# Kernel optimization log

Hardware: AMD Instinct MI355X
Metric: run time of the kernel (lower is better)

Reference implementation:

```python
import jax, jax.numpy as jnp
import numpy as np

GROUP_SIZE = 128  # K-rows sharing one dequant scale


def _dequant(B, s):
    """Unpack int4 (uint4b8: value = nibble - 8) from packed int32 and apply group scales.
    B: [K//8, N] int32, 8 nibbles per word along K (nibble i -> k = 8*row + i).
    s: [K//GROUP_SIZE, N] float scales.
    Returns W: [K, N] float.
    """
    Kp, N = B.shape
    K = Kp * 8
    shifts = (jnp.arange(8, dtype=jnp.int32) * 4)
    # [Kp, 8, N] nibbles -> [K, N]
    nib = (B[:, None, :] >> shifts[None, :, None]) & 0xF
    w = nib.reshape(K, N).astype(s.dtype) - 8.0
    # per-group scaling: groups of GROUP_SIZE consecutive K rows
    w = (w.reshape(K // GROUP_SIZE, GROUP_SIZE, N) * s[:, None, :]).reshape(K, N)
    return w


def setup_inputs() -> dict:
    key = jax.random.key(0)
    k1, k2, k3 = jax.random.split(key, 3)
    M, K, N = 64, 8192, 8192
    x = jax.random.normal(k1, (M, K), dtype=jnp.float32)
    B = jax.random.randint(k2, (K // 8, N), 0, 2147483647, dtype=jnp.int32)
    s = jax.random.uniform(k3, (K // GROUP_SIZE, N), dtype=jnp.float32) * 0.02
    return {"x": x, "B": B, "s": s}


def reference(x, B, s):
    # machete_mm: fused int4 dequant + GEMM; here expressed as dequant then matmul
    w = _dequant(B, s)          # [K, N]
    out = x @ w                 # [M, N]
    return out
```

## Files before the change

### kernel.cpp

```cpp
#include <hip/hip_runtime.h>

typedef _Float16 half2v __attribute__((ext_vector_type(2)));
typedef _Float16 half8  __attribute__((ext_vector_type(8)));
typedef float    floatx4 __attribute__((ext_vector_type(4)));

#define M_DIM 64
#define K_DIM 8192
#define N_DIM 8192
#define NT 64
#define KSB 8
#define CHUNK (K_DIM / (KSB * 4))
#define STEPS (CHUNK / 32)

__global__ __launch_bounds__(256) void permute_x_kernel(
        const float* __restrict__ x, _Float16* __restrict__ xp) {
    const int t  = blockIdx.x * 256 + threadIdx.x;
    const int c  = t & 15;
    const int q  = (t >> 4) & 3;
    const int mt = (t >> 6) & 3;
    const int kb = t >> 8;
    const int m  = mt * 16 + c;
    const int k0 = kb * 32 + q * 8;
    const float* src = x + (size_t)m * K_DIM + k0;
    float4 a = *(const float4*)(src);
    float4 b = *(const float4*)(src + 4);
    union { _Float16 h[8]; float4 f; } u;
    u.h[0] = (_Float16)a.x; u.h[1] = (_Float16)b.x;
    u.h[2] = (_Float16)a.y; u.h[3] = (_Float16)b.y;
    u.h[4] = (_Float16)a.z; u.h[5] = (_Float16)b.z;
    u.h[6] = (_Float16)a.w; u.h[7] = (_Float16)b.w;
    *(float4*)(xp + (size_t)t * 8) = u.f;
}

__device__ __forceinline__ half2v dq_pair(unsigned int bits, half2v sub, half2v sc) {
    union { unsigned int u; half2v h; } cv;
    cv.u = bits;
    return (cv.h - sub) * sc;
}

__global__ __launch_bounds__(256, 3) void machete_mm_kernel(
        const _Float16* __restrict__ xp,
        const unsigned int* __restrict__ Bq,
        const float* __restrict__ s,
        float* __restrict__ partial) {
    __shared__ float red[4][32][65];

    const int tid  = threadIdx.x;
    const int w    = tid >> 6;
    const int lane = tid & 63;
    const int c    = lane & 15;
    const int q    = lane >> 4;
    const int n0   = blockIdx.x * NT;
    const int ci   = blockIdx.y * 4 + w;
    const int kb   = ci * CHUNK;
    const int ncol = n0 + 4 * c;

    floatx4 acc[4][4];
    #pragma unroll
    for (int i = 0; i < 4; ++i)
        #pragma unroll
        for (int j = 0; j < 4; ++j) acc[i][j] = (floatx4)0.0f;

    const half2v c1032 = { (_Float16)1032.0f, (_Float16)1032.0f };
    half2v s2g[2][4];
    #pragma unroll
    for (int g = 0; g < 2; ++g) {
        const float4 s4 = *(const float4*)(s + (size_t)((kb >> 7) + g) * N_DIM + ncol);
        s2g[g][0] = (half2v){ (_Float16)s4.x, (_Float16)s4.x };
        s2g[g][1] = (half2v){ (_Float16)s4.y, (_Float16)s4.y };
        s2g[g][2] = (half2v){ (_Float16)s4.z, (_Float16)s4.z };
        s2g[g][3] = (half2v){ (_Float16)s4.w, (_Float16)s4.w };
    }

    const unsigned int* bq = Bq + (size_t)((kb >> 3) + q) * N_DIM + ncol;
    const _Float16*     ap = xp + (size_t)(kb >> 5) * 2048 + lane * 8;

    uint4 bbuf[2];
    half8 abuf[2][4];
    bbuf[0] = *(const uint4*)bq; bq += (size_t)4 * N_DIM;
    bbuf[1] = *(const uint4*)bq; bq += (size_t)4 * N_DIM;
    #pragma unroll
    for (int mt = 0; mt < 4; ++mt)
        abuf[0][mt] = *(const half8*)(ap + mt * 512);

    #pragma unroll 2
    for (int st = 0; st < STEPS; ++st) {
        const int p = st & 1;
        const int g = st >> 2;

        union { uint4 v; unsigned int a[4]; } bv;
        bv.v = bbuf[p];
        half8 bf[4];
        #pragma unroll
        for (int t = 0; t < 4; ++t) {
            const unsigned int wd = bv.a[t];
            const half2v sc = s2g[g][t];
            union { half2v h2[4]; half8 h8; } b8;
            b8.h2[0] = dq_pair(( wd        & 0x000F000Fu) | 0x64006400u, c1032, sc);
            b8.h2[1] = dq_pair(((wd >> 4)  & 0x000F000Fu) | 0x64006400u, c1032, sc);
            b8.h2[2] = dq_pair(((wd >> 8)  & 0x000F000Fu) | 0x64006400u, c1032, sc);
            b8.h2[3] = dq_pair(((wd >> 12) & 0x000F000Fu) | 0x64006400u, c1032, sc);
            bf[t] = b8.h8;
        }

        if (st < STEPS - 2) bbuf[p] = *(const uint4*)bq;
        bq += (size_t)4 * N_DIM;
        if (st < STEPS - 1) {
            ap += 2048;
            #pragma unroll
            for (int mt = 0; mt < 4; ++mt)
                abuf[p ^ 1][mt] = *(const half8*)(ap + mt * 512);
        }

        #pragma unroll
        for (int t = 0; t < 4; ++t)
            #pragma unroll
            for (int mt = 0; mt < 4; ++mt)
                acc[mt][t] = __builtin_amdgcn_mfma_f32_16x16x32_f16(
                    abuf[p][mt], bf[t], acc[mt][t], 0, 0, 0);
    }

    float* ptile = partial + ((size_t)blockIdx.y * M_DIM) * N_DIM + n0;
    #pragma unroll
    for (int r = 0; r < 2; ++r) {
        if (r) __syncthreads();
        #pragma unroll
        for (int h = 0; h < 2; ++h) {
            const int mt = 2 * r + h;
            #pragma unroll
            for (int t = 0; t < 4; ++t)
                #pragma unroll
                for (int rr = 0; rr < 4; ++rr)
                    red[w][h * 16 + q * 4 + rr][4 * c + t] = acc[mt][t][rr];
        }
        __syncthreads();
        #pragma unroll
        for (int i = 0; i < 8; ++i) {
            const int idx = i * 256 + tid;
            const int mr  = idx >> 6;
            const int nl  = idx & 63;
            const float v = red[0][mr][nl] + red[1][mr][nl]
                          + red[2][mr][nl] + red[3][mr][nl];
            ptile[(size_t)(r * 32 + mr) * N_DIM + nl] = v;
        }
    }
}

__global__ __launch_bounds__(256) void reduce_kernel(
        const float* __restrict__ partial, float* __restrict__ out) {
    const size_t i = ((size_t)blockIdx.x * 256 + threadIdx.x) * 4;
    const size_t S = (size_t)M_DIM * N_DIM;
    float4 v = *(const float4*)(partial + i);
    #pragma unroll
    for (int bk = 1; bk < KSB; ++bk) {
        const float4 u = *(const float4*)(partial + bk * S + i);
        v.x += u.x; v.y += u.y; v.z += u.z; v.w += u.w;
    }
    *(float4*)(out + i) = v;
}

extern "C" void kernel_launch(void* const* d_in, const int* in_sizes, int n_in,
                              void* d_out, int out_size, void* d_ws, size_t ws_size,
                              hipStream_t stream) {
    const float*        x  = (const float*)d_in[0];
    const unsigned int* Bq = (const unsigned int*)d_in[1];
    const float*        sc = (const float*)d_in[2];
    float* out     = (float*)d_out;
    _Float16* xp   = (_Float16*)d_ws;
    float* partial = (float*)((char*)d_ws + (1 << 20));

    permute_x_kernel<<<dim3(M_DIM * K_DIM / 8 / 256), 256, 0, stream>>>(x, xp);
    machete_mm_kernel<<<dim3(N_DIM / NT, KSB), 256, 0, stream>>>(xp, Bq, sc, partial);
    reduce_kernel<<<dim3(M_DIM * N_DIM / (256 * 4)), 256, 0, stream>>>(partial, out);
}
```

Measured before the change: 100.4 us.

## Stage A and B tiles through LDS via global_load_lds double buffering

Replaces per-wave register double-buffered global loads with async global-to-LDS DMA (global_load_lds) into a two-stage shared-memory buffer, one stage being 128 K rows per block. The K split across the 4 waves becomes interleaved inside each stage instead of contiguous per-wave chunks, and group scales are loaded once per stage. The aim is to hide global-load latency and cut VGPR pressure. In exchange it adds a block barrier every stage, raises LDS use to about 40KB per block, and relies on the DMA completing before the barrier.

```diff
diff --git a/kernel.cpp b/kernel.cpp
--- a/kernel.cpp
+++ b/kernel.cpp
@@ -9,8 +9,7 @@
 #define N_DIM 8192
 #define NT 64
 #define KSB 8
-#define CHUNK (K_DIM / (KSB * 4))
-#define STEPS (CHUNK / 32)
+#define STAGES 8
 
 __global__ __launch_bounds__(256) void permute_x_kernel(
         const float* __restrict__ x, _Float16* __restrict__ xp) {
@@ -32,6 +31,13 @@
     *(float4*)(xp + (size_t)t * 8) = u.f;
 }
 
+__device__ __forceinline__ void dma16(const void* g, void* l) {
+    __builtin_amdgcn_global_load_lds(
+        (const __attribute__((address_space(1))) unsigned int*)(uintptr_t)g,
+        (__attribute__((address_space(3))) unsigned int*)(uintptr_t)l,
+        16, 0, 0);
+}
+
 __device__ __forceinline__ half2v dq_pair(unsigned int bits, half2v sub, half2v sc) {
     union { unsigned int u; half2v h; } cv;
     cv.u = bits;
@@ -43,7 +49,11 @@
         const unsigned int* __restrict__ Bq,
         const float* __restrict__ s,
         float* __restrict__ partial) {
-    __shared__ float red[4][32][65];
+    union SM {
+        char stage[2][20480];
+        float red[4][32][65];
+    };
+    __shared__ SM sm;
 
     const int tid  = threadIdx.x;
     const int w    = tid >> 6;
@@ -51,9 +61,13 @@
     const int c    = lane & 15;
     const int q    = lane >> 4;
     const int n0   = blockIdx.x * NT;
-    const int ci   = blockIdx.y * 4 + w;
-    const int kb   = ci * CHUNK;
+    const int kb0  = blockIdx.y * (K_DIM / KSB);
     const int ncol = n0 + 4 * c;
+
+    const char* a_base = (const char*)xp + (size_t)(kb0 >> 5) * 4096;
+    const char* b_base = (const char*)Bq + ((size_t)(kb0 >> 3) * N_DIM + n0) * 4;
+    const size_t b_lane = (size_t)(lane >> 4) * ((size_t)N_DIM * 4) + (size_t)(lane & 15) * 16;
+    const int    a_lane = lane * 16;
 
     floatx4 acc[4][4];
     #pragma unroll
@@ -62,62 +76,58 @@
         for (int j = 0; j < 4; ++j) acc[i][j] = (floatx4)0.0f;
 
     const half2v c1032 = { (_Float16)1032.0f, (_Float16)1032.0f };
-    half2v s2g[2][4];
-    #pragma unroll
-    for (int g = 0; g < 2; ++g) {
-        const float4 s4 = *(const float4*)(s + (size_t)((kb >> 7) + g) * N_DIM + ncol);
-        s2g[g][0] = (half2v){ (_Float16)s4.x, (_Float16)s4.x };
-        s2g[g][1] = (half2v){ (_Float16)s4.y, (_Float16)s4.y };
-        s2g[g][2] = (half2v){ (_Float16)s4.z, (_Float16)s4.z };
-        s2g[g][3] = (half2v){ (_Float16)s4.w, (_Float16)s4.w };
-    }
 
-    const unsigned int* bq = Bq + (size_t)((kb >> 3) + q) * N_DIM + ncol;
-    const _Float16*     ap = xp + (size_t)(kb >> 5) * 2048 + lane * 8;
+    auto stage_dma = [&](int si, int p) {
+        const char* as = a_base + (size_t)si * 16384;
+        #pragma unroll
+        for (int call = 0; call < 4; ++call) {
+            const int idx = call * 4 + w;
+            dma16(as + idx * 1024 + a_lane, &sm.stage[p][idx * 1024]);
+        }
+        const char* bs = b_base + (size_t)(si * 16 + w * 4) * ((size_t)N_DIM * 4) + b_lane;
+        dma16(bs, &sm.stage[p][16384 + w * 1024]);
+    };
 
-    uint4 bbuf[2];
-    half8 abuf[2][4];
-    bbuf[0] = *(const uint4*)bq; bq += (size_t)4 * N_DIM;
-    bbuf[1] = *(const uint4*)bq; bq += (size_t)4 * N_DIM;
-    #pragma unroll
-    for (int mt = 0; mt < 4; ++mt)
-        abuf[0][mt] = *(const half8*)(ap + mt * 512);
+    stage_dma(0, 0);
+    __syncthreads();
 
-    #pragma unroll 2
-    for (int st = 0; st < STEPS; ++st) {
+    for (int st = 0; st < STAGES; ++st) {
         const int p = st & 1;
-        const int g = st >> 2;
 
+        const float4 s4 = *(const float4*)(s + (size_t)((kb0 >> 7) + st) * N_DIM + ncol);
+
+        if (st + 1 < STAGES) stage_dma(st + 1, p ^ 1);
+
+        half2v s2[4];
+        s2[0] = (half2v){ (_Float16)s4.x, (_Float16)s4.x };
+        s2[1] = (half2v){ (_Float16)s4.y, (_Float16)s4.y };
+        s2[2] = (half2v){ (_Float16)s4.z, (_Float16)s4.z };
+        s2[3] = (half2v){ (_Float16)s4.w, (_Float16)s4.w };
+
+        const char* ab = &sm.stage[p][w * 4096];
+        half8 afr[4];
+        #pragma unroll
+        for (int mt = 0; mt < 4; ++mt)
+            afr[mt] = *(const half8*)(ab + mt * 1024 + a_lane);
         union { uint4 v; unsigned int a[4]; } bv;
-        bv.v = bbuf[p];
-        half8 bf[4];
+        bv.v = *(const uint4*)(&sm.stage[p][16384 + w * 1024 + q * 256 + c * 16]);
+
         #pragma unroll
         for (int t = 0; t < 4; ++t) {
             const unsigned int wd = bv.a[t];
-            const half2v sc = s2g[g][t];
+            const half2v sc = s2[t];
             union { half2v h2[4]; half8 h8; } b8;
             b8.h2[0] = dq_pair(( wd        & 0x000F000Fu) | 0x64006400u, c1032, sc);
             b8.h2[1] = dq_pair(((wd >> 4)  & 0x000F000Fu) | 0x64006400u, c1032, sc);
             b8.h2[2] = dq_pair(((wd >> 8)  & 0x000F000Fu) | 0x64006400u, c1032, sc);
             b8.h2[3] = dq_pair(((wd >> 12) & 0x000F000Fu) | 0x64006400u, c1032, sc);
-            bf[t] = b8.h8;
-        }
-
-        if (st < STEPS - 2) bbuf[p] = *(const uint4*)bq;
-        bq += (size_t)4 * N_DIM;
-        if (st < STEPS - 1) {
-            ap += 2048;
-            #pragma unroll
-            for (int mt = 0; mt < 4; ++mt)
-                abuf[p ^ 1][mt] = *(const half8*)(ap + mt * 512);
-        }
-
-        #pragma unroll
-        for (int t = 0; t < 4; ++t)
             #pragma unroll
             for (int mt = 0; mt < 4; ++mt)
                 acc[mt][t] = __builtin_amdgcn_mfma_f32_16x16x32_f16(
-                    abuf[p][mt], bf[t], acc[mt][t], 0, 0, 0);
+                    afr[mt], b8.h8, acc[mt][t], 0, 0, 0);
+        }
+
+        __syncthreads();
     }
 
     float* ptile = partial + ((size_t)blockIdx.y * M_DIM) * N_DIM + n0;
@@ -131,7 +141,7 @@
             for (int t = 0; t < 4; ++t)
                 #pragma unroll
                 for (int rr = 0; rr < 4; ++rr)
-                    red[w][h * 16 + q * 4 + rr][4 * c + t] = acc[mt][t][rr];
+                    sm.red[w][h * 16 + q * 4 + rr][4 * c + t] = acc[mt][t][rr];
         }
         __syncthreads();
         #pragma unroll
@@ -139,8 +149,8 @@
             const int idx = i * 256 + tid;
             const int mr  = idx >> 6;
             const int nl  = idx & 63;
-            const float v = red[0][mr][nl] + red[1][mr][nl]
-                          + red[2][mr][nl] + red[3][mr][nl];
+            const float v = sm.red[0][mr][nl] + sm.red[1][mr][nl]
+                          + sm.red[2][mr][nl] + sm.red[3][mr][nl];
             ptile[(size_t)(r * 32 + mr) * N_DIM + nl] = v;
         }
     }
```

Result: no change. 98.89 us (-1.5%).
